# Performance work log

Measured on AMD Instinct MI355X. Metric: run time of the kernel, lower is better.

Reference implementation:

```python
import jax, jax.numpy as jnp
import numpy as np

STAGE_NUM = 3
EPS = 1e-6
BN_EPS = 1e-5


def setup_inputs() -> dict:
    key = jax.random.key(0)
    ks = jax.random.split(key, 6)
    b, c, h, w, k = 16, 512, 64, 64, 64
    x = jax.random.normal(ks[0], (b, c, h, w), dtype=jnp.float32)
    conv1_w = jax.random.normal(ks[1], (c, c), dtype=jnp.float32) * np.sqrt(2.0 / c)
    conv1_b = jax.random.normal(ks[2], (c,), dtype=jnp.float32) * 0.01
    mu = jax.random.normal(ks[3], (c, k), dtype=jnp.float32) * np.sqrt(2.0 / k)
    mu = mu / (EPS + jnp.linalg.norm(mu, axis=0, keepdims=True))
    conv2_w = jax.random.normal(ks[4], (c, c), dtype=jnp.float32) * np.sqrt(2.0 / c)
    bn_gamma = jnp.ones((c,), dtype=jnp.float32)
    bn_beta = jnp.zeros((c,), dtype=jnp.float32)
    bn_mean = jnp.zeros((c,), dtype=jnp.float32)
    bn_var = jnp.ones((c,), dtype=jnp.float32)
    return {"x": x, "conv1_w": conv1_w, "conv1_b": conv1_b, "mu": mu,
            "conv2_w": conv2_w, "bn_gamma": bn_gamma, "bn_beta": bn_beta,
            "bn_mean": bn_mean, "bn_var": bn_var}


def _l2norm(a, axis):
    return a / (EPS + jnp.linalg.norm(a, axis=axis, keepdims=True))


def reference(x, conv1_w, conv1_b, mu, conv2_w, bn_gamma, bn_beta, bn_mean, bn_var):
    b, c, h, w = x.shape
    n = h * w
    # conv1: 1x1 conv with bias == per-pixel matmul
    x = jnp.einsum('oc,bchw->bohw', conv1_w, x) + conv1_b[None, :, None, None]
    xf = x.reshape(b, c, n)             # (b, c, n)
    x_t = xf.transpose(0, 2, 1)         # (b, n, c)
    m = mu                              # (c, k), broadcast on first iter
    z = None
    for _ in range(STAGE_NUM):
        z = jax.nn.softmax(jnp.matmul(x_t, m), axis=2)        # (b, n, k)
        z_ = z / (EPS + z.sum(axis=1, keepdims=True))          # column-normalize
        m = jnp.matmul(xf, z_)                                 # (b, c, k)
        m = _l2norm(m, axis=1)
    # EM loop is under torch.no_grad in the original
    m = jax.lax.stop_gradient(m)
    z = jax.lax.stop_gradient(z)
    rec = jnp.matmul(m, z.transpose(0, 2, 1))                  # (b, c, n)
    rec = jax.nn.relu(rec).reshape(b, c, h, w)
    # conv2: 1x1 conv (no bias) + BatchNorm (inference form, running stats)
    out = jnp.einsum('oc,bchw->bohw', conv2_w, rec)
    inv = bn_gamma / jnp.sqrt(bn_var + BN_EPS)
    out = out * inv[None, :, None, None] + (bn_beta - bn_mean * inv)[None, :, None, None]
    return out
```

## Files before the change

### kernel.cpp

```cpp
#include <hip/hip_runtime.h>
#include <stdint.h>

#define BB 16
#define CC 512
#define NN 4096
#define KC 64

typedef unsigned short ushort_t;
typedef __attribute__((ext_vector_type(8))) __bf16 bf16x8;
typedef __attribute__((ext_vector_type(4))) float f32x4;

static __device__ __forceinline__ float bu2f(ushort_t u){
  union{unsigned int i; float f;} v; v.i = ((unsigned int)u)<<16; return v.f;
}
static __device__ __forceinline__ ushort_t f2bu(float f){
  unsigned int x = __float_as_uint(f);
  return (ushort_t)((x + 0x7FFFu + ((x>>16)&1u)) >> 16);
}
static __device__ __forceinline__ ushort_t lo_part(float v, ushort_t hi){
  return f2bu(v - bu2f(hi));
}

#define MFMA16(a,b,c) __builtin_amdgcn_mfma_f32_16x16x32_bf16(a,b,c,0,0,0)

template<int ROWS>
static __device__ __forceinline__ void stage32(const ushort_t* __restrict__ g, int ld,
                                               ushort_t* l, int tid){
  int wid = tid >> 6, lane = tid & 63;
  #pragma unroll
  for (int it = 0; it < ROWS/64; ++it){
    int chunk = it*4 + wid;
    int row = chunk*16 + (lane >> 2);
    int seg = (lane & 3) ^ ((row >> 1) & 3);
    const ushort_t* gp = g + (size_t)row*ld + seg*8;
    ushort_t* lp = l + chunk*512;
    __builtin_amdgcn_global_load_lds(
        (const __attribute__((address_space(1))) void*)gp,
        (__attribute__((address_space(3))) void*)lp, 16, 0, 0);
  }
}
static __device__ __forceinline__ bf16x8 frag32(const ushort_t* l, int row, int ko){
  return *(const bf16x8*)(l + row*32 + (ko ^ (((row >> 1) & 3) << 3)));
}

__global__ __launch_bounds__(256) void k_transpose(const float* __restrict__ x,
    ushort_t* __restrict__ xTh, ushort_t* __restrict__ xTl, int hasLo){
  __shared__ ushort_t th[64][68];
  __shared__ ushort_t tl[64][68];
  int b = blockIdx.z, c0 = blockIdx.y*64, n0 = blockIdx.x*64;
  int r16 = threadIdx.x >> 4;
  int q4  = (threadIdx.x & 15) * 4;
  #pragma unroll
  for (int p = 0; p < 4; ++p){
    int row = r16 + p*16;
    size_t off = ((size_t)b*CC + c0 + row)*NN + n0 + q4;
    float4 v = *(const float4*)(x + off);
    ushort_t h0=f2bu(v.x), h1=f2bu(v.y), h2=f2bu(v.z), h3=f2bu(v.w);
    th[q4+0][row]=h0; th[q4+1][row]=h1; th[q4+2][row]=h2; th[q4+3][row]=h3;
    if (hasLo){
      tl[q4+0][row]=lo_part(v.x,h0); tl[q4+1][row]=lo_part(v.y,h1);
      tl[q4+2][row]=lo_part(v.z,h2); tl[q4+3][row]=lo_part(v.w,h3);
    }
  }
  __syncthreads();
  #pragma unroll
  for (int p = 0; p < 4; ++p){
    int nrow = r16 + p*16;
    size_t off = ((size_t)b*NN + n0 + nrow)*CC + c0 + q4;
    ushort4 v;
    v.x = th[nrow][q4+0]; v.y = th[nrow][q4+1]; v.z = th[nrow][q4+2]; v.w = th[nrow][q4+3];
    *(ushort4*)(xTh + off) = v;
    if (hasLo){
      ushort4 u;
      u.x = tl[nrow][q4+0]; u.y = tl[nrow][q4+1]; u.z = tl[nrow][q4+2]; u.w = tl[nrow][q4+3];
      *(ushort4*)(xTl + off) = u;
    }
  }
}

__global__ __launch_bounds__(256) void k_prep(const float* __restrict__ gamma,
    const float* __restrict__ beta, const float* __restrict__ mean,
    const float* __restrict__ var, const float* __restrict__ b1,
    const float* __restrict__ W1, const float* __restrict__ W2,
    const float* __restrict__ mu,
    float* __restrict__ bnscale, float* __restrict__ bnshift,
    float* __restrict__ b1f,
    ushort_t* __restrict__ W1h, ushort_t* __restrict__ W1l,
    ushort_t* __restrict__ W2h, ushort_t* __restrict__ W2l,
    ushort_t* __restrict__ mTh, ushort_t* __restrict__ mTl){
  int t = blockIdx.x*256 + threadIdx.x;
  if (t < CC){
    float inv = gamma[t] * rsqrtf(var[t] + 1e-5f);
    bnscale[t] = inv;
    bnshift[t] = beta[t] - mean[t]*inv;
    b1f[t] = b1[t];
  }
  if (t < CC*CC){
    float w1 = W1[t], w2 = W2[t];
    ushort_t h1 = f2bu(w1), h2 = f2bu(w2);
    W1h[t] = h1; W1l[t] = lo_part(w1,h1);
    W2h[t] = h2; W2l[t] = lo_part(w2,h2);
  }
  if (t < BB*KC*CC){
    int c = t & (CC-1);
    int k = (t >> 9) & (KC-1);
    float v = mu[(size_t)c*KC + k];
    ushort_t h = f2bu(v);
    mTh[t] = h; mTl[t] = lo_part(v,h);
  }
}

__global__ __launch_bounds__(256) void k_conv1(const ushort_t* __restrict__ W1h,
    const ushort_t* __restrict__ W1l, const float* __restrict__ bias,
    const ushort_t* __restrict__ xTh, const ushort_t* __restrict__ xTl, int hasBl,
    ushort_t* __restrict__ xfh, ushort_t* __restrict__ xfl, int hasxfl,
    ushort_t* __restrict__ xt1h, ushort_t* __restrict__ xt1l, int hasxt1l){
  __shared__ __align__(16) ushort_t sm[16896];
  ushort_t* lAh = sm;
  ushort_t* lAl = sm + 4096;
  ushort_t* lBh = sm + 8192;
  ushort_t* lBl = sm + 12288;
  int b = blockIdx.z, m0 = blockIdx.y*128, n0 = blockIdx.x*128;
  int tid = threadIdx.x, wid = tid>>6, lane = tid&63, quad = lane>>4, l16 = lane&15;
  int wm = wid>>1, wn = wid&1;
  f32x4 zero4 = {0.f,0.f,0.f,0.f};
  f32x4 acc[4][4];
  #pragma unroll
  for (int i=0;i<4;++i){
    #pragma unroll
    for (int j=0;j<4;++j) acc[i][j] = zero4;
  }
  const ushort_t* Aph = W1h + (size_t)m0*CC;
  const ushort_t* Apl = W1l + (size_t)m0*CC;
  const ushort_t* Bph = xTh + ((size_t)b*NN + n0)*CC;
  const ushort_t* Bpl = hasBl ? xTl + ((size_t)b*NN + n0)*CC : nullptr;
  for (int k0 = 0; k0 < CC; k0 += 32){
    stage32<128>(Aph + k0, CC, lAh, tid);
    stage32<128>(Apl + k0, CC, lAl, tid);
    stage32<128>(Bph + k0, CC, lBh, tid);
    if (hasBl) stage32<128>(Bpl + k0, CC, lBl, tid);
    __syncthreads();
    {
      bf16x8 ah[4], al[4], bh[4], bl[4];
      #pragma unroll
      for (int f=0; f<4; ++f){
        ah[f] = frag32(lAh, wm*64 + f*16 + l16, quad*8);
        al[f] = frag32(lAl, wm*64 + f*16 + l16, quad*8);
        bh[f] = frag32(lBh, wn*64 + f*16 + l16, quad*8);
      }
      if (hasBl){
        #pragma unroll
        for (int f=0; f<4; ++f) bl[f] = frag32(lBl, wn*64 + f*16 + l16, quad*8);
      }
      #pragma unroll
      for (int i=0;i<4;++i){
        #pragma unroll
        for (int j=0;j<4;++j){
          acc[i][j] = MFMA16(ah[i], bh[j], acc[i][j]);
          acc[i][j] = MFMA16(al[i], bh[j], acc[i][j]);
        }
      }
      if (hasBl){
        #pragma unroll
        for (int i=0;i<4;++i){
          #pragma unroll
          for (int j=0;j<4;++j) acc[i][j] = MFMA16(ah[i], bl[j], acc[i][j]);
        }
      }
    }
    __syncthreads();
  }
  ushort_t* ct = sm;
  float vals[4][4][4];
  #pragma unroll
  for (int i=0;i<4;++i){
    #pragma unroll
    for (int r=0;r<4;++r){
      int m = wm*64 + i*16 + quad*4 + r;
      float bv = bias[m0 + m];
      #pragma unroll
      for (int j=0;j<4;++j){
        float v = acc[i][j][r] + bv;
        vals[i][j][r] = v;
        ct[m*132 + (wn*64 + j*16 + l16)] = f2bu(v);
      }
    }
  }
  __syncthreads();
  {
    ushort_t* xfp = xfh + (size_t)b*CC*NN + (size_t)m0*NN + n0;
    #pragma unroll
    for (int i = 0; i < 16; ++i){
      int idx = tid + i*256;
      int m = idx >> 5, j4 = (idx & 31)*4;
      *(ushort4*)(xfp + (size_t)m*NN + j4) = *(ushort4*)(ct + m*132 + j4);
    }
    ushort_t* xtp = xt1h + ((size_t)b*NN + n0)*CC + m0;
    #pragma unroll
    for (int i = 0; i < 16; ++i){
      int idx = tid + i*256;
      int nrow = idx >> 5, c4 = (idx & 31)*4;
      ushort4 v;
      v.x = ct[(c4+0)*132 + nrow]; v.y = ct[(c4+1)*132 + nrow];
      v.z = ct[(c4+2)*132 + nrow]; v.w = ct[(c4+3)*132 + nrow];
      *(ushort4*)(xtp + (size_t)nrow*CC + c4) = v;
    }
  }
  if (hasxfl || hasxt1l){
    __syncthreads();
    #pragma unroll
    for (int i=0;i<4;++i){
      #pragma unroll
      for (int r=0;r<4;++r){
        int m = wm*64 + i*16 + quad*4 + r;
        #pragma unroll
        for (int j=0;j<4;++j){
          float v = vals[i][j][r];
          ct[m*132 + (wn*64 + j*16 + l16)] = lo_part(v, f2bu(v));
        }
      }
    }
    __syncthreads();
    if (hasxfl){
      ushort_t* xfp = xfl + (size_t)b*CC*NN + (size_t)m0*NN + n0;
      #pragma unroll
      for (int i = 0; i < 16; ++i){
        int idx = tid + i*256;
        int m = idx >> 5, j4 = (idx & 31)*4;
        *(ushort4*)(xfp + (size_t)m*NN + j4) = *(ushort4*)(ct + m*132 + j4);
      }
    }
    if (hasxt1l){
      ushort_t* xtp = xt1l + ((size_t)b*NN + n0)*CC + m0;
      #pragma unroll
      for (int i = 0; i < 16; ++i){
        int idx = tid + i*256;
        int nrow = idx >> 5, c4 = (idx & 31)*4;
        ushort4 v;
        v.x = ct[(c4+0)*132 + nrow]; v.y = ct[(c4+1)*132 + nrow];
        v.z = ct[(c4+2)*132 + nrow]; v.w = ct[(c4+3)*132 + nrow];
        *(ushort4*)(xtp + (size_t)nrow*CC + c4) = v;
      }
    }
  }
}

__global__ __launch_bounds__(256) void k_logits(const ushort_t* __restrict__ xt1h,
    const ushort_t* __restrict__ xt1l, int hasAl,
    const ushort_t* __restrict__ mTh, const ushort_t* __restrict__ mTl,
    ushort_t* __restrict__ zh, ushort_t* __restrict__ zl,
    ushort_t* __restrict__ zTh, ushort_t* __restrict__ zTl,
    float* __restrict__ colsum){
  __shared__ __align__(16) ushort_t sm[12288];
  ushort_t* lAh = sm;
  ushort_t* lAl = sm + 4096;
  ushort_t* lBh = sm + 8192;
  ushort_t* lBl = sm + 10240;
  int b = blockIdx.y, n0 = blockIdx.x*128;
  int tid = threadIdx.x, wid = tid>>6, lane = tid&63, quad = lane>>4, l16 = lane&15;
  f32x4 zero4 = {0.f,0.f,0.f,0.f};
  f32x4 acc[2][4];
  #pragma unroll
  for (int i=0;i<2;++i){
    #pragma unroll
    for (int j=0;j<4;++j) acc[i][j] = zero4;
  }
  const ushort_t* Aph = xt1h + ((size_t)b*NN + n0)*CC;
  const ushort_t* Apl = hasAl ? xt1l + ((size_t)b*NN + n0)*CC : nullptr;
  const ushort_t* Bph = mTh + (size_t)b*KC*CC;
  const ushort_t* Bpl = mTl + (size_t)b*KC*CC;
  for (int k0 = 0; k0 < CC; k0 += 32){
    stage32<128>(Aph + k0, CC, lAh, tid);
    if (hasAl) stage32<128>(Apl + k0, CC, lAl, tid);
    stage32<64>(Bph + k0, CC, lBh, tid);
    stage32<64>(Bpl + k0, CC, lBl, tid);
    __syncthreads();
    {
      bf16x8 ah[2], al[2], bh[4], bl[4];
      #pragma unroll
      for (int f=0; f<2; ++f){
        ah[f] = frag32(lAh, wid*32 + f*16 + l16, quad*8);
        if (hasAl) al[f] = frag32(lAl, wid*32 + f*16 + l16, quad*8);
      }
      #pragma unroll
      for (int f=0; f<4; ++f){
        bh[f] = frag32(lBh, f*16 + l16, quad*8);
        bl[f] = frag32(lBl, f*16 + l16, quad*8);
      }
      #pragma unroll
      for (int i=0;i<2;++i){
        #pragma unroll
        for (int j=0;j<4;++j){
          acc[i][j] = MFMA16(ah[i], bh[j], acc[i][j]);
          acc[i][j] = MFMA16(ah[i], bl[j], acc[i][j]);
        }
      }
      if (hasAl){
        #pragma unroll
        for (int i=0;i<2;++i){
          #pragma unroll
          for (int j=0;j<4;++j) acc[i][j] = MFMA16(al[i], bh[j], acc[i][j]);
        }
      }
    }
    __syncthreads();
  }
  #pragma unroll
  for (int i=0;i<2;++i){
    #pragma unroll
    for (int r=0;r<4;++r){
      float mx = fmaxf(fmaxf(acc[i][0][r], acc[i][1][r]), fmaxf(acc[i][2][r], acc[i][3][r]));
      mx = fmaxf(mx, __shfl_xor(mx, 1));
      mx = fmaxf(mx, __shfl_xor(mx, 2));
      mx = fmaxf(mx, __shfl_xor(mx, 4));
      mx = fmaxf(mx, __shfl_xor(mx, 8));
      float e0 = __expf(acc[i][0][r]-mx), e1 = __expf(acc[i][1][r]-mx);
      float e2 = __expf(acc[i][2][r]-mx), e3 = __expf(acc[i][3][r]-mx);
      float s = e0+e1+e2+e3;
      s += __shfl_xor(s, 1); s += __shfl_xor(s, 2);
      s += __shfl_xor(s, 4); s += __shfl_xor(s, 8);
      float inv = 1.0f/s;
      acc[i][0][r] = e0*inv; acc[i][1][r] = e1*inv;
      acc[i][2][r] = e2*inv; acc[i][3][r] = e3*inv;
    }
  }
  #pragma unroll
  for (int j=0;j<4;++j){
    float p = 0.f;
    #pragma unroll
    for (int i=0;i<2;++i){
      #pragma unroll
      for (int r=0;r<4;++r) p += acc[i][j][r];
    }
    p += __shfl_xor(p, 16); p += __shfl_xor(p, 32);
    if (lane < 16) atomicAdd(&colsum[b*KC + j*16 + l16], p);
  }
  #pragma unroll
  for (int i=0;i<2;++i){
    int nbase = wid*32 + i*16 + quad*4;
    #pragma unroll
    for (int j=0;j<4;++j){
      int k = j*16 + l16;
      ushort4 vh, vl;
      float a0=acc[i][j][0], a1=acc[i][j][1], a2=acc[i][j][2], a3=acc[i][j][3];
      vh.x=f2bu(a0); vh.y=f2bu(a1); vh.z=f2bu(a2); vh.w=f2bu(a3);
      vl.x=lo_part(a0,vh.x); vl.y=lo_part(a1,vh.y); vl.z=lo_part(a2,vh.z); vl.w=lo_part(a3,vh.w);
      size_t zoff = ((size_t)b*KC + k)*NN + n0 + nbase;
      *(ushort4*)(zTh + zoff) = vh;
      *(ushort4*)(zTl + zoff) = vl;
      const ushort_t* ph = (const ushort_t*)&vh;
      const ushort_t* pl = (const ushort_t*)&vl;
      #pragma unroll
      for (int r=0;r<4;++r){
        size_t o = ((size_t)b*NN + n0 + nbase + r)*KC + k;
        zh[o] = ph[r]; zl[o] = pl[r];
      }
    }
  }
}

__global__ __launch_bounds__(256) void k_mgemm(const ushort_t* __restrict__ xfh,
    const ushort_t* __restrict__ xfl, int hasAl,
    const ushort_t* __restrict__ zTh, const ushort_t* __restrict__ zTl,
    float* __restrict__ m_part){
  __shared__ __align__(16) ushort_t sm[12288];
  ushort_t* lAh = sm;
  ushort_t* lAl = sm + 4096;
  ushort_t* lBh = sm + 8192;
  ushort_t* lBl = sm + 10240;
  int c0 = blockIdx.x*128, slice = blockIdx.y, b = blockIdx.z;
  int tid = threadIdx.x, wid = tid>>6, lane = tid&63, quad = lane>>4, l16 = lane&15;
  f32x4 zero4 = {0.f,0.f,0.f,0.f};
  f32x4 acc[2][4];
  #pragma unroll
  for (int i=0;i<2;++i){
    #pragma unroll
    for (int j=0;j<4;++j) acc[i][j] = zero4;
  }
  const ushort_t* Aph = xfh + ((size_t)b*CC + c0)*NN + slice*512;
  const ushort_t* Apl = hasAl ? xfl + ((size_t)b*CC + c0)*NN + slice*512 : nullptr;
  const ushort_t* Bph = zTh + (size_t)b*KC*NN + slice*512;
  const ushort_t* Bpl = zTl + (size_t)b*KC*NN + slice*512;
  for (int k0 = 0; k0 < 512; k0 += 32){
    stage32<128>(Aph + k0, NN, lAh, tid);
    if (hasAl) stage32<128>(Apl + k0, NN, lAl, tid);
    stage32<64>(Bph + k0, NN, lBh, tid);
    stage32<64>(Bpl + k0, NN, lBl, tid);
    __syncthreads();
    {
      bf16x8 ah[2], al[2], bh[4], bl[4];
      #pragma unroll
      for (int f=0; f<2; ++f){
        ah[f] = frag32(lAh, wid*32 + f*16 + l16, quad*8);
        if (hasAl) al[f] = frag32(lAl, wid*32 + f*16 + l16, quad*8);
      }
      #pragma unroll
      for (int f=0; f<4; ++f){
        bh[f] = frag32(lBh, f*16 + l16, quad*8);
        bl[f] = frag32(lBl, f*16 + l16, quad*8);
      }
      #pragma unroll
      for (int i=0;i<2;++i){
        #pragma unroll
        for (int j=0;j<4;++j){
          acc[i][j] = MFMA16(ah[i], bh[j], acc[i][j]);
          acc[i][j] = MFMA16(ah[i], bl[j], acc[i][j]);
        }
      }
      if (hasAl){
        #pragma unroll
        for (int i=0;i<2;++i){
          #pragma unroll
          for (int j=0;j<4;++j) acc[i][j] = MFMA16(al[i], bh[j], acc[i][j]);
        }
      }
    }
    __syncthreads();
  }
  #pragma unroll
  for (int i=0;i<2;++i){
    int c = c0 + wid*32 + i*16 + quad*4;
    #pragma unroll
    for (int j=0;j<4;++j){
      int k = j*16 + l16;
      *(f32x4*)(m_part + (((size_t)slice*BB + b)*KC + k)*CC + c) = acc[i][j];
    }
  }
}

__global__ __launch_bounds__(256) void k_mnorm(const float* __restrict__ m_part,
    const float* __restrict__ colsum,
    ushort_t* __restrict__ mch, ushort_t* __restrict__ mcl,
    ushort_t* __restrict__ mTh, ushort_t* __restrict__ mTl){
  int k = blockIdx.x, b = blockIdx.y, t = threadIdx.x;
  float v0 = 0.f, v1 = 0.f;
  #pragma unroll
  for (int s = 0; s < 8; ++s){
    const float* p = m_part + (((size_t)s*BB + b)*KC + k)*CC;
    v0 += p[t]; v1 += p[t+256];
  }
  float sk = 1.0f/(1e-6f + colsum[b*KC + k]);
  v0 *= sk; v1 *= sk;
  float ss = v0*v0 + v1*v1;
  #pragma unroll
  for (int off = 1; off < 64; off <<= 1) ss += __shfl_xor(ss, off);
  __shared__ float red[4];
  if ((t&63) == 0) red[t>>6] = ss;
  __syncthreads();
  float inv = 1.0f/(1e-6f + sqrtf(red[0]+red[1]+red[2]+red[3]));
  v0 *= inv; v1 *= inv;
  ushort_t h0 = f2bu(v0), h1 = f2bu(v1);
  ushort_t l0 = lo_part(v0,h0), l1 = lo_part(v1,h1);
  size_t to = ((size_t)b*KC + k)*CC + t;
  mTh[to] = h0; mTh[to+256] = h1;
  mTl[to] = l0; mTl[to+256] = l1;
  size_t co = ((size_t)b*CC + t)*KC + k;
  mch[co] = h0; mch[co + (size_t)256*KC] = h1;
  mcl[co] = l0; mcl[co + (size_t)256*KC] = l1;
}

__global__ __launch_bounds__(256) void k_rec(const ushort_t* __restrict__ zh,
    const ushort_t* __restrict__ zl,
    const ushort_t* __restrict__ mch, const ushort_t* __restrict__ mcl,
    ushort_t* __restrict__ recTh, ushort_t* __restrict__ recTl){
  __shared__ __align__(16) ushort_t sm[16896];
  ushort_t* lAh = sm;
  ushort_t* lAl = sm + 4096;
  ushort_t* lBh = sm + 8192;
  ushort_t* lBl = sm + 12288;
  int n0 = blockIdx.x*128, c0 = blockIdx.y*128, b = blockIdx.z;
  int tid = threadIdx.x, wid = tid>>6, lane = tid&63, quad = lane>>4, l16 = lane&15;
  int wm = wid>>1, wn = wid&1;
  f32x4 zero4 = {0.f,0.f,0.f,0.f};
  f32x4 acc[4][4];
  #pragma unroll
  for (int i=0;i<4;++i){
    #pragma unroll
    for (int j=0;j<4;++j) acc[i][j] = zero4;
  }
  const ushort_t* Aph = zh + ((size_t)b*NN + n0)*KC;
  const ushort_t* Apl = zl + ((size_t)b*NN + n0)*KC;
  const ushort_t* Bph = mch + ((size_t)b*CC + c0)*KC;
  const ushort_t* Bpl = mcl + ((size_t)b*CC + c0)*KC;
  for (int k0 = 0; k0 < KC; k0 += 32){
    stage32<128>(Aph + k0, KC, lAh, tid);
    stage32<128>(Apl + k0, KC, lAl, tid);
    stage32<128>(Bph + k0, KC, lBh, tid);
    stage32<128>(Bpl + k0, KC, lBl, tid);
    __syncthreads();
    {
      bf16x8 ah[4], al[4], bh[4], bl[4];
      #pragma unroll
      for (int f=0; f<4; ++f){
        ah[f] = frag32(lAh, wm*64 + f*16 + l16, quad*8);
        al[f] = frag32(lAl, wm*64 + f*16 + l16, quad*8);
        bh[f] = frag32(lBh, wn*64 + f*16 + l16, quad*8);
        bl[f] = frag32(lBl, wn*64 + f*16 + l16, quad*8);
      }
      #pragma unroll
      for (int i=0;i<4;++i){
        #pragma unroll
        for (int j=0;j<4;++j){
          acc[i][j] = MFMA16(ah[i], bh[j], acc[i][j]);
          acc[i][j] = MFMA16(ah[i], bl[j], acc[i][j]);
          acc[i][j] = MFMA16(al[i], bh[j], acc[i][j]);
        }
      }
    }
    __syncthreads();
  }
  ushort_t* ct = sm;
  #pragma unroll
  for (int i=0;i<4;++i){
    #pragma unroll
    for (int r=0;r<4;++r){
      int m = wm*64 + i*16 + quad*4 + r;
      #pragma unroll
      for (int j=0;j<4;++j)
        ct[m*132 + (wn*64 + j*16 + l16)] = f2bu(fmaxf(acc[i][j][r], 0.f));
    }
  }
  __syncthreads();
  {
    ushort_t* rp = recTh + ((size_t)b*NN + n0)*CC + c0;
    #pragma unroll
    for (int i = 0; i < 16; ++i){
      int idx = tid + i*256;
      int m = idx >> 5, j4 = (idx & 31)*4;
      *(ushort4*)(rp + (size_t)m*CC + j4) = *(ushort4*)(ct + m*132 + j4);
    }
  }
  __syncthreads();
  #pragma unroll
  for (int i=0;i<4;++i){
    #pragma unroll
    for (int r=0;r<4;++r){
      int m = wm*64 + i*16 + quad*4 + r;
      #pragma unroll
      for (int j=0;j<4;++j){
        float v = fmaxf(acc[i][j][r], 0.f);
        ct[m*132 + (wn*64 + j*16 + l16)] = lo_part(v, f2bu(v));
      }
    }
  }
  __syncthreads();
  {
    ushort_t* rp = recTl + ((size_t)b*NN + n0)*CC + c0;
    #pragma unroll
    for (int i = 0; i < 16; ++i){
      int idx = tid + i*256;
      int m = idx >> 5, j4 = (idx & 31)*4;
      *(ushort4*)(rp + (size_t)m*CC + j4) = *(ushort4*)(ct + m*132 + j4);
    }
  }
}

__global__ __launch_bounds__(256) void k_conv2(const ushort_t* __restrict__ W2h,
    const ushort_t* __restrict__ W2l,
    const ushort_t* __restrict__ recTh, const ushort_t* __restrict__ recTl,
    const float* __restrict__ bnscale, const float* __restrict__ bnshift,
    float* __restrict__ out){
  __shared__ __align__(16) ushort_t sm[16384];
  ushort_t* lAh = sm;
  ushort_t* lAl = sm + 4096;
  ushort_t* lBh = sm + 8192;
  ushort_t* lBl = sm + 12288;
  int b = blockIdx.z, m0 = blockIdx.y*128, n0 = blockIdx.x*128;
  int tid = threadIdx.x, wid = tid>>6, lane = tid&63, quad = lane>>4, l16 = lane&15;
  int wm = wid>>1, wn = wid&1;
  f32x4 zero4 = {0.f,0.f,0.f,0.f};
  f32x4 acc[4][4];
  #pragma unroll
  for (int i=0;i<4;++i){
    #pragma unroll
    for (int j=0;j<4;++j) acc[i][j] = zero4;
  }
  const ushort_t* Aph = W2h + (size_t)m0*CC;
  const ushort_t* Apl = W2l + (size_t)m0*CC;
  const ushort_t* Bph = recTh + ((size_t)b*NN + n0)*CC;
  const ushort_t* Bpl = recTl + ((size_t)b*NN + n0)*CC;
  for (int k0 = 0; k0 < CC; k0 += 32){
    stage32<128>(Aph + k0, CC, lAh, tid);
    stage32<128>(Apl + k0, CC, lAl, tid);
    stage32<128>(Bph + k0, CC, lBh, tid);
    stage32<128>(Bpl + k0, CC, lBl, tid);
    __syncthreads();
    {
      bf16x8 ah[4], al[4], bh[4], bl[4];
      #pragma unroll
      for (int f=0; f<4; ++f){
        ah[f] = frag32(lAh, wm*64 + f*16 + l16, quad*8);
        al[f] = frag32(lAl, wm*64 + f*16 + l16, quad*8);
        bh[f] = frag32(lBh, wn*64 + f*16 + l16, quad*8);
        bl[f] = frag32(lBl, wn*64 + f*16 + l16, quad*8);
      }
      #pragma unroll
      for (int i=0;i<4;++i){
        #pragma unroll
        for (int j=0;j<4;++j){
          acc[i][j] = MFMA16(ah[i], bh[j], acc[i][j]);
          acc[i][j] = MFMA16(ah[i], bl[j], acc[i][j]);
          acc[i][j] = MFMA16(al[i], bh[j], acc[i][j]);
        }
      }
    }
    __syncthreads();
  }
  size_t base = (size_t)b*CC*NN;
  #pragma unroll
  for (int i=0;i<4;++i){
    #pragma unroll
    for (int r=0;r<4;++r){
      int m = m0 + wm*64 + i*16 + quad*4 + r;
      float sc = bnscale[m], sh = bnshift[m];
      #pragma unroll
      for (int j=0;j<4;++j){
        int nn = n0 + wn*64 + j*16 + l16;
        out[base + (size_t)m*NN + nn] = acc[i][j][r]*sc + sh;
      }
    }
  }
}

extern "C" void kernel_launch(void* const* d_in, const int* in_sizes, int n_in,
                              void* d_out, int out_size, void* d_ws, size_t ws_size,
                              hipStream_t stream) {
  (void)in_sizes; (void)n_in; (void)out_size;
  const float* x     = (const float*)d_in[0];
  const float* W1    = (const float*)d_in[1];
  const float* b1    = (const float*)d_in[2];
  const float* mu    = (const float*)d_in[3];
  const float* W2    = (const float*)d_in[4];
  const float* gamma = (const float*)d_in[5];
  const float* beta  = (const float*)d_in[6];
  const float* mean  = (const float*)d_in[7];
  const float* var   = (const float*)d_in[8];
  float* out = (float*)d_out;

  const size_t big = (size_t)BB*NN*CC*2;
  const size_t zsz = (size_t)BB*NN*KC*2;
  char* w = (char*)d_ws;
  ushort_t* xTh  = (ushort_t*)w;  w += big;
  ushort_t* zh   = xTh;
  ushort_t* zl   = (ushort_t*)((char*)xTh + zsz);
  ushort_t* zTh  = (ushort_t*)((char*)xTh + 2*zsz);
  ushort_t* zTl  = (ushort_t*)((char*)xTh + 3*zsz);
  float*    m_part = (float*)((char*)xTh + 4*zsz);
  ushort_t* xfh  = (ushort_t*)w;  w += big;
  ushort_t* xt1h = (ushort_t*)w;  w += big;
  ushort_t* mTh  = (ushort_t*)w;  w += (size_t)BB*KC*CC*2;
  ushort_t* mTl  = (ushort_t*)w;  w += (size_t)BB*KC*CC*2;
  ushort_t* mch  = (ushort_t*)w;  w += (size_t)BB*KC*CC*2;
  ushort_t* mcl  = (ushort_t*)w;  w += (size_t)BB*KC*CC*2;
  ushort_t* W1h  = (ushort_t*)w;  w += (size_t)CC*CC*2;
  ushort_t* W1l  = (ushort_t*)w;  w += (size_t)CC*CC*2;
  ushort_t* W2h  = (ushort_t*)w;  w += (size_t)CC*CC*2;
  ushort_t* W2l  = (ushort_t*)w;  w += (size_t)CC*CC*2;
  float*    bnscale = (float*)w;  w += 2048;
  float*    bnshift = (float*)w;  w += 2048;
  float*    b1f  = (float*)w;     w += 2048;
  float*    colsum = (float*)w;   w += (size_t)BB*KC*4;
  ushort_t* xTl = nullptr; ushort_t* xt1l = nullptr; ushort_t* xfl = nullptr;
  size_t used = (size_t)(w - (char*)d_ws);
  if (used + big <= ws_size){ xTl  = (ushort_t*)w; w += big; used += big; }
  if (used + big <= ws_size){ xt1l = (ushort_t*)w; w += big; used += big; }
  if (used + big <= ws_size){ xfl  = (ushort_t*)w; w += big; used += big; }
  int hasxTl = xTl != nullptr, hasxt1l = xt1l != nullptr, hasxfl = xfl != nullptr;
  ushort_t* recTh = xt1h;
  ushort_t* recTl = hasxt1l ? xt1l : xfh;

  k_transpose<<<dim3(NN/64, CC/64, BB), 256, 0, stream>>>(x, xTh, xTl, hasxTl);
  k_prep<<<dim3((BB*KC*CC + 255)/256), 256, 0, stream>>>(gamma, beta, mean, var, b1,
      W1, W2, mu, bnscale, bnshift, b1f, W1h, W1l, W2h, W2l, mTh, mTl);
  k_conv1<<<dim3(NN/128, CC/128, BB), 256, 0, stream>>>(W1h, W1l, b1f, xTh, xTl, hasxTl,
      xfh, xfl, hasxfl, xt1h, xt1l, hasxt1l);
  for (int it = 0; it < 3; ++it){
    (void)hipMemsetAsync(colsum, 0, (size_t)BB*KC*4, stream);
    k_logits<<<dim3(NN/128, BB), 256, 0, stream>>>(xt1h, xt1l, hasxt1l, mTh, mTl,
        zh, zl, zTh, zTl, colsum);
    k_mgemm<<<dim3(CC/128, 8, BB), 256, 0, stream>>>(xfh, xfl, hasxfl, zTh, zTl, m_part);
    k_mnorm<<<dim3(KC, BB), 256, 0, stream>>>(m_part, colsum, mch, mcl, mTh, mTl);
  }
  k_rec<<<dim3(NN/128, CC/128, BB), 256, 0, stream>>>(zh, zl, mch, mcl, recTh, recTl);
  k_conv2<<<dim3(NN/128, CC/128, BB), 256, 0, stream>>>(W2h, W2l, recTh, recTl,
      bnscale, bnshift, out);
}
```

Measured before the change: 874.2 us.

## Double-buffer LDS staging in all GEMM kernels to overlap loads with MFMA

```diff
diff --git a/kernel.cpp b/kernel.cpp
--- a/kernel.cpp
+++ b/kernel.cpp
@@ -115,11 +115,7 @@
     const ushort_t* __restrict__ xTh, const ushort_t* __restrict__ xTl, int hasBl,
     ushort_t* __restrict__ xfh, ushort_t* __restrict__ xfl, int hasxfl,
     ushort_t* __restrict__ xt1h, ushort_t* __restrict__ xt1l, int hasxt1l){
-  __shared__ __align__(16) ushort_t sm[16896];
-  ushort_t* lAh = sm;
-  ushort_t* lAl = sm + 4096;
-  ushort_t* lBh = sm + 8192;
-  ushort_t* lBl = sm + 12288;
+  __shared__ __align__(16) ushort_t sm[32768];
   int b = blockIdx.z, m0 = blockIdx.y*128, n0 = blockIdx.x*128;
   int tid = threadIdx.x, wid = tid>>6, lane = tid&63, quad = lane>>4, l16 = lane&15;
   int wm = wid>>1, wn = wid&1;
@@ -134,38 +130,44 @@
   const ushort_t* Apl = W1l + (size_t)m0*CC;
   const ushort_t* Bph = xTh + ((size_t)b*NN + n0)*CC;
   const ushort_t* Bpl = hasBl ? xTl + ((size_t)b*NN + n0)*CC : nullptr;
-  for (int k0 = 0; k0 < CC; k0 += 32){
-    stage32<128>(Aph + k0, CC, lAh, tid);
-    stage32<128>(Apl + k0, CC, lAl, tid);
-    stage32<128>(Bph + k0, CC, lBh, tid);
-    if (hasBl) stage32<128>(Bpl + k0, CC, lBl, tid);
-    __syncthreads();
-    {
-      bf16x8 ah[4], al[4], bh[4], bl[4];
-      #pragma unroll
-      for (int f=0; f<4; ++f){
-        ah[f] = frag32(lAh, wm*64 + f*16 + l16, quad*8);
-        al[f] = frag32(lAl, wm*64 + f*16 + l16, quad*8);
-        bh[f] = frag32(lBh, wn*64 + f*16 + l16, quad*8);
-      }
-      if (hasBl){
-        #pragma unroll
-        for (int f=0; f<4; ++f) bl[f] = frag32(lBl, wn*64 + f*16 + l16, quad*8);
-      }
+  auto stage_all = [&](int buf, int k0){
+    ushort_t* base = sm + buf*16384;
+    stage32<128>(Aph + k0, CC, base,         tid);
+    stage32<128>(Apl + k0, CC, base + 4096,  tid);
+    stage32<128>(Bph + k0, CC, base + 8192,  tid);
+    if (hasBl) stage32<128>(Bpl + k0, CC, base + 12288, tid);
+  };
+  stage_all(0, 0);
+  __syncthreads();
+  const int NSTEP = CC/32;
+  for (int s = 0; s < NSTEP; ++s){
+    int cur = s & 1;
+    if (s+1 < NSTEP) stage_all(cur^1, (s+1)*32);
+    ushort_t* base = sm + cur*16384;
+    bf16x8 ah[4], al[4], bh[4], bl[4];
+    #pragma unroll
+    for (int f=0; f<4; ++f){
+      ah[f] = frag32(base,         wm*64 + f*16 + l16, quad*8);
+      al[f] = frag32(base + 4096,  wm*64 + f*16 + l16, quad*8);
+      bh[f] = frag32(base + 8192,  wn*64 + f*16 + l16, quad*8);
+    }
+    if (hasBl){
+      #pragma unroll
+      for (int f=0; f<4; ++f) bl[f] = frag32(base + 12288, wn*64 + f*16 + l16, quad*8);
+    }
+    #pragma unroll
+    for (int i=0;i<4;++i){
+      #pragma unroll
+      for (int j=0;j<4;++j){
+        acc[i][j] = MFMA16(ah[i], bh[j], acc[i][j]);
+        acc[i][j] = MFMA16(al[i], bh[j], acc[i][j]);
+      }
+    }
+    if (hasBl){
       #pragma unroll
       for (int i=0;i<4;++i){
         #pragma unroll
-        for (int j=0;j<4;++j){
-          acc[i][j] = MFMA16(ah[i], bh[j], acc[i][j]);
-          acc[i][j] = MFMA16(al[i], bh[j], acc[i][j]);
-        }
-      }
-      if (hasBl){
-        #pragma unroll
-        for (int i=0;i<4;++i){
-          #pragma unroll
-          for (int j=0;j<4;++j) acc[i][j] = MFMA16(ah[i], bl[j], acc[i][j]);
-        }
+        for (int j=0;j<4;++j) acc[i][j] = MFMA16(ah[i], bl[j], acc[i][j]);
       }
     }
     __syncthreads();
@@ -251,11 +253,7 @@
     ushort_t* __restrict__ zh, ushort_t* __restrict__ zl,
     ushort_t* __restrict__ zTh, ushort_t* __restrict__ zTl,
     float* __restrict__ colsum){
-  __shared__ __align__(16) ushort_t sm[12288];
-  ushort_t* lAh = sm;
-  ushort_t* lAl = sm + 4096;
-  ushort_t* lBh = sm + 8192;
-  ushort_t* lBl = sm + 10240;
+  __shared__ __align__(16) ushort_t sm[24576];
   int b = blockIdx.y, n0 = blockIdx.x*128;
   int tid = threadIdx.x, wid = tid>>6, lane = tid&63, quad = lane>>4, l16 = lane&15;
   f32x4 zero4 = {0.f,0.f,0.f,0.f};
@@ -269,38 +267,44 @@
   const ushort_t* Apl = hasAl ? xt1l + ((size_t)b*NN + n0)*CC : nullptr;
   const ushort_t* Bph = mTh + (size_t)b*KC*CC;
   const ushort_t* Bpl = mTl + (size_t)b*KC*CC;
-  for (int k0 = 0; k0 < CC; k0 += 32){
-    stage32<128>(Aph + k0, CC, lAh, tid);
-    if (hasAl) stage32<128>(Apl + k0, CC, lAl, tid);
-    stage32<64>(Bph + k0, CC, lBh, tid);
-    stage32<64>(Bpl + k0, CC, lBl, tid);
-    __syncthreads();
-    {
-      bf16x8 ah[2], al[2], bh[4], bl[4];
-      #pragma unroll
-      for (int f=0; f<2; ++f){
-        ah[f] = frag32(lAh, wid*32 + f*16 + l16, quad*8);
-        if (hasAl) al[f] = frag32(lAl, wid*32 + f*16 + l16, quad*8);
-      }
-      #pragma unroll
-      for (int f=0; f<4; ++f){
-        bh[f] = frag32(lBh, f*16 + l16, quad*8);
-        bl[f] = frag32(lBl, f*16 + l16, quad*8);
-      }
+  auto stage_all = [&](int buf, int k0){
+    ushort_t* base = sm + buf*12288;
+    stage32<128>(Aph + k0, CC, base,         tid);
+    if (hasAl) stage32<128>(Apl + k0, CC, base + 4096, tid);
+    stage32<64>(Bph + k0, CC, base + 8192,  tid);
+    stage32<64>(Bpl + k0, CC, base + 10240, tid);
+  };
+  stage_all(0, 0);
+  __syncthreads();
+  const int NSTEP = CC/32;
+  for (int s = 0; s < NSTEP; ++s){
+    int cur = s & 1;
+    if (s+1 < NSTEP) stage_all(cur^1, (s+1)*32);
+    ushort_t* base = sm + cur*12288;
+    bf16x8 ah[2], al[2], bh[4], bl[4];
+    #pragma unroll
+    for (int f=0; f<2; ++f){
+      ah[f] = frag32(base, wid*32 + f*16 + l16, quad*8);
+      if (hasAl) al[f] = frag32(base + 4096, wid*32 + f*16 + l16, quad*8);
+    }
+    #pragma unroll
+    for (int f=0; f<4; ++f){
+      bh[f] = frag32(base + 8192,  f*16 + l16, quad*8);
+      bl[f] = frag32(base + 10240, f*16 + l16, quad*8);
+    }
+    #pragma unroll
+    for (int i=0;i<2;++i){
+      #pragma unroll
+      for (int j=0;j<4;++j){
+        acc[i][j] = MFMA16(ah[i], bh[j], acc[i][j]);
+        acc[i][j] = MFMA16(ah[i], bl[j], acc[i][j]);
+      }
+    }
+    if (hasAl){
       #pragma unroll
       for (int i=0;i<2;++i){
         #pragma unroll
-        for (int j=0;j<4;++j){
-          acc[i][j] = MFMA16(ah[i], bh[j], acc[i][j]);
-          acc[i][j] = MFMA16(ah[i], bl[j], acc[i][j]);
-        }
-      }
-      if (hasAl){
-        #pragma unroll
-        for (int i=0;i<2;++i){
-          #pragma unroll
-          for (int j=0;j<4;++j) acc[i][j] = MFMA16(al[i], bh[j], acc[i][j]);
-        }
+        for (int j=0;j<4;++j) acc[i][j] = MFMA16(al[i], bh[j], acc[i][j]);
       }
     }
     __syncthreads();
@@ -363,11 +367,7 @@
     const ushort_t* __restrict__ xfl, int hasAl,
     const ushort_t* __restrict__ zTh, const ushort_t* __restrict__ zTl,
     float* __restrict__ m_part){
-  __shared__ __align__(16) ushort_t sm[12288];
-  ushort_t* lAh = sm;
-  ushort_t* lAl = sm + 4096;
-  ushort_t* lBh = sm + 8192;
-  ushort_t* lBl = sm + 10240;
+  __shared__ __align__(16) ushort_t sm[24576];
   int c0 = blockIdx.x*128, slice = blockIdx.y, b = blockIdx.z;
   int tid = threadIdx.x, wid = tid>>6, lane = tid&63, quad = lane>>4, l16 = lane&15;
   f32x4 zero4 = {0.f,0.f,0.f,0.f};
@@ -381,38 +381,44 @@
   const ushort_t* Apl = hasAl ? xfl + ((size_t)b*CC + c0)*NN + slice*512 : nullptr;
   const ushort_t* Bph = zTh + (size_t)b*KC*NN + slice*512;
   const ushort_t* Bpl = zTl + (size_t)b*KC*NN + slice*512;
-  for (int k0 = 0; k0 < 512; k0 += 32){
-    stage32<128>(Aph + k0, NN, lAh, tid);
-    if (hasAl) stage32<128>(Apl + k0, NN, lAl, tid);
-    stage32<64>(Bph + k0, NN, lBh, tid);
-    stage32<64>(Bpl + k0, NN, lBl, tid);
-    __syncthreads();
-    {
-      bf16x8 ah[2], al[2], bh[4], bl[4];
-      #pragma unroll
-      for (int f=0; f<2; ++f){
-        ah[f] = frag32(lAh, wid*32 + f*16 + l16, quad*8);
-        if (hasAl) al[f] = frag32(lAl, wid*32 + f*16 + l16, quad*8);
-      }
-      #pragma unroll
-      for (int f=0; f<4; ++f){
-        bh[f] = frag32(lBh, f*16 + l16, quad*8);
-        bl[f] = frag32(lBl, f*16 + l16, quad*8);
-      }
+  auto stage_all = [&](int buf, int k0){
+    ushort_t* base = sm + buf*12288;
+    stage32<128>(Aph + k0, NN, base,         tid);
+    if (hasAl) stage32<128>(Apl + k0, NN, base + 4096, tid);
+    stage32<64>(Bph + k0, NN, base + 8192,  tid);
+    stage32<64>(Bpl + k0, NN, base + 10240, tid);
+  };
+  stage_all(0, 0);
+  __syncthreads();
+  const int NSTEP = 512/32;
+  for (int s = 0; s < NSTEP; ++s){
+    int cur = s & 1;
+    if (s+1 < NSTEP) stage_all(cur^1, (s+1)*32);
+    ushort_t* base = sm + cur*12288;
+    bf16x8 ah[2], al[2], bh[4], bl[4];
+    #pragma unroll
+    for (int f=0; f<2; ++f){
+      ah[f] = frag32(base, wid*32 + f*16 + l16, quad*8);
+      if (hasAl) al[f] = frag32(base + 4096, wid*32 + f*16 + l16, quad*8);
+    }
+    #pragma unroll
+    for (int f=0; f<4; ++f){
+      bh[f] = frag32(base + 8192,  f*16 + l16, quad*8);
+      bl[f] = frag32(base + 10240, f*16 + l16, quad*8);
+    }
+    #pragma unroll
+    for (int i=0;i<2;++i){
+      #pragma unroll
+      for (int j=0;j<4;++j){
+        acc[i][j] = MFMA16(ah[i], bh[j], acc[i][j]);
+        acc[i][j] = MFMA16(ah[i], bl[j], acc[i][j]);
+      }
+    }
+    if (hasAl){
       #pragma unroll
       for (int i=0;i<2;++i){
         #pragma unroll
-        for (int j=0;j<4;++j){
-          acc[i][j] = MFMA16(ah[i], bh[j], acc[i][j]);
-          acc[i][j] = MFMA16(ah[i], bl[j], acc[i][j]);
-        }
-      }
-      if (hasAl){
-        #pragma unroll
-        for (int i=0;i<2;++i){
-          #pragma unroll
-          for (int j=0;j<4;++j) acc[i][j] = MFMA16(al[i], bh[j], acc[i][j]);
-        }
+        for (int j=0;j<4;++j) acc[i][j] = MFMA16(al[i], bh[j], acc[i][j]);
       }
     }
     __syncthreads();
@@ -463,11 +469,7 @@
     const ushort_t* __restrict__ zl,
     const ushort_t* __restrict__ mch, const ushort_t* __restrict__ mcl,
     ushort_t* __restrict__ recTh, ushort_t* __restrict__ recTl){
-  __shared__ __align__(16) ushort_t sm[16896];
-  ushort_t* lAh = sm;
-  ushort_t* lAl = sm + 4096;
-  ushort_t* lBh = sm + 8192;
-  ushort_t* lBl = sm + 12288;
+  __shared__ __align__(16) ushort_t sm[32768];
   int n0 = blockIdx.x*128, c0 = blockIdx.y*128, b = blockIdx.z;
   int tid = threadIdx.x, wid = tid>>6, lane = tid&63, quad = lane>>4, l16 = lane&15;
   int wm = wid>>1, wn = wid&1;
@@ -482,29 +484,35 @@
   const ushort_t* Apl = zl + ((size_t)b*NN + n0)*KC;
   const ushort_t* Bph = mch + ((size_t)b*CC + c0)*KC;
   const ushort_t* Bpl = mcl + ((size_t)b*CC + c0)*KC;
-  for (int k0 = 0; k0 < KC; k0 += 32){
-    stage32<128>(Aph + k0, KC, lAh, tid);
-    stage32<128>(Apl + k0, KC, lAl, tid);
-    stage32<128>(Bph + k0, KC, lBh, tid);
-    stage32<128>(Bpl + k0, KC, lBl, tid);
-    __syncthreads();
-    {
-      bf16x8 ah[4], al[4], bh[4], bl[4];
-      #pragma unroll
-      for (int f=0; f<4; ++f){
-        ah[f] = frag32(lAh, wm*64 + f*16 + l16, quad*8);
-        al[f] = frag32(lAl, wm*64 + f*16 + l16, quad*8);
-        bh[f] = frag32(lBh, wn*64 + f*16 + l16, quad*8);
-        bl[f] = frag32(lBl, wn*64 + f*16 + l16, quad*8);
-      }
-      #pragma unroll
-      for (int i=0;i<4;++i){
-        #pragma unroll
-        for (int j=0;j<4;++j){
-          acc[i][j] = MFMA16(ah[i], bh[j], acc[i][j]);
-          acc[i][j] = MFMA16(ah[i], bl[j], acc[i][j]);
-          acc[i][j] = MFMA16(al[i], bh[j], acc[i][j]);
-        }
+  auto stage_all = [&](int buf, int k0){
+    ushort_t* base = sm + buf*16384;
+    stage32<128>(Aph + k0, KC, base,         tid);
+    stage32<128>(Apl + k0, KC, base + 4096,  tid);
+    stage32<128>(Bph + k0, KC, base + 8192,  tid);
+    stage32<128>(Bpl + k0, KC, base + 12288, tid);
+  };
+  stage_all(0, 0);
+  __syncthreads();
+  const int NSTEP = KC/32;
+  for (int s = 0; s < NSTEP; ++s){
+    int cur = s & 1;
+    if (s+1 < NSTEP) stage_all(cur^1, (s+1)*32);
+    ushort_t* base = sm + cur*16384;
+    bf16x8 ah[4], al[4], bh[4], bl[4];
+    #pragma unroll
+    for (int f=0; f<4; ++f){
+      ah[f] = frag32(base,         wm*64 + f*16 + l16, quad*8);
+      al[f] = frag32(base + 4096,  wm*64 + f*16 + l16, quad*8);
+      bh[f] = frag32(base + 8192,  wn*64 + f*16 + l16, quad*8);
+      bl[f] = frag32(base + 12288, wn*64 + f*16 + l16, quad*8);
+    }
+    #pragma unroll
+    for (int i=0;i<4;++i){
+      #pragma unroll
+      for (int j=0;j<4;++j){
+        acc[i][j] = MFMA16(ah[i], bh[j], acc[i][j]);
+        acc[i][j] = MFMA16(ah[i], bl[j], acc[i][j]);
+        acc[i][j] = MFMA16(al[i], bh[j], acc[i][j]);
       }
     }
     __syncthreads();
@@ -560,11 +568,7 @@
     const ushort_t* __restrict__ recTh, const ushort_t* __restrict__ recTl,
     const float* __restrict__ bnscale, const float* __restrict__ bnshift,
     float* __restrict__ out){
-  __shared__ __align__(16) ushort_t sm[16384];
-  ushort_t* lAh = sm;
-  ushort_t* lAl = sm + 4096;
-  ushort_t* lBh = sm + 8192;
-  ushort_t* lBl = sm + 12288;
+  __shared__ __align__(16) ushort_t sm[32768];
   int b = blockIdx.z, m0 = blockIdx.y*128, n0 = blockIdx.x*128;
   int tid = threadIdx.x, wid = tid>>6, lane = tid&63, quad = lane>>4, l16 = lane&15;
   int wm = wid>>1, wn = wid&1;
@@ -579,29 +583,35 @@
   const ushort_t* Apl = W2l + (size_t)m0*CC;
   const ushort_t* Bph = recTh + ((size_t)b*NN + n0)*CC;
   const ushort_t* Bpl = recTl + ((size_t)b*NN + n0)*CC;
-  for (int k0 = 0; k0 < CC; k0 += 32){
-    stage32<128>(Aph + k0, CC, lAh, tid);
-    stage32<128>(Apl + k0, CC, lAl, tid);
-    stage32<128>(Bph + k0, CC, lBh, tid);
-    stage32<128>(Bpl + k0, CC, lBl, tid);
-    __syncthreads();
-    {
-      bf16x8 ah[4], al[4], bh[4], bl[4];
-      #pragma unroll
-      for (int f=0; f<4; ++f){
-        ah[f] = frag32(lAh, wm*64 + f*16 + l16, quad*8);
-        al[f] = frag32(lAl, wm*64 + f*16 + l16, quad*8);
-        bh[f] = frag32(lBh, wn*64 + f*16 + l16, quad*8);
-        bl[f] = frag32(lBl, wn*64 + f*16 + l16, quad*8);
-      }
-      #pragma unroll
-      for (int i=0;i<4;++i){
-        #pragma unroll
-        for (int j=0;j<4;++j){
-          acc[i][j] = MFMA16(ah[i], bh[j], acc[i][j]);
-          acc[i][j] = MFMA16(ah[i], bl[j], acc[i][j]);
-          acc[i][j] = MFMA16(al[i], bh[j], acc[i][j]);
-        }
+  auto stage_all = [&](int buf, int k0){
+    ushort_t* base = sm + buf*16384;
+    stage32<128>(Aph + k0, CC, base,         tid);
+    stage32<128>(Apl + k0, CC, base + 4096,  tid);
+    stage32<128>(Bph + k0, CC, base + 8192,  tid);
+    stage32<128>(Bpl + k0, CC, base + 12288, tid);
+  };
+  stage_all(0, 0);
+  __syncthreads();
+  const int NSTEP = CC/32;
+  for (int s = 0; s < NSTEP; ++s){
+    int cur = s & 1;
+    if (s+1 < NSTEP) stage_all(cur^1, (s+1)*32);
+    ushort_t* base = sm + cur*16384;
+    bf16x8 ah[4], al[4], bh[4], bl[4];
+    #pragma unroll
+    for (int f=0; f<4; ++f){
+      ah[f] = frag32(base,         wm*64 + f*16 + l16, quad*8);
+      al[f] = frag32(base + 4096,  wm*64 + f*16 + l16, quad*8);
+      bh[f] = frag32(base + 8192,  wn*64 + f*16 + l16, quad*8);
+      bl[f] = frag32(base + 12288, wn*64 + f*16 + l16, quad*8);
+    }
+    #pragma unroll
+    for (int i=0;i<4;++i){
+      #pragma unroll
+      for (int j=0;j<4;++j){
+        acc[i][j] = MFMA16(ah[i], bh[j], acc[i][j]);
+        acc[i][j] = MFMA16(ah[i], bl[j], acc[i][j]);
+        acc[i][j] = MFMA16(al[i], bh[j], acc[i][j]);
       }
     }
     __syncthreads();
```

Measured after the change: 901.2 us. 3.1% more time.
